# Kernel optimization log

Hardware: AMD Instinct MI355X
Metric: run time of the kernel (lower is better)

## Reference

```python
import jax, jax.numpy as jnp
import numpy as np


def setup_inputs() -> dict:
    key = jax.random.key(0)
    ks = jax.random.split(key, 10)
    B, T, D = 256, 256, 256
    CH, L, K = 128, 3, 10          # chunk_size, levels, conv_size
    H = CH * L                     # hidden_dim = 384
    G = 4 * H + 2 * L              # gate projection width = 1542
    HS = H // 6

    def xavier(k, shape):
        fan_in, fan_out = shape[0], shape[-1]
        lim = np.sqrt(6.0 / (fan_in + fan_out)).astype(np.float32)
        return jax.random.uniform(k, shape, jnp.float32, -lim, lim)

    x = jax.random.normal(ks[0], (B, T, D), jnp.float32)
    lengths = jax.random.randint(ks[1], (B,), 1, T + 1).astype(jnp.int64)
    Wk = xavier(ks[2], (D + 1, G)); bk = jnp.zeros((G,), jnp.float32)
    Wr = xavier(ks[3], (H + 1, G)); br = jnp.zeros((G,), jnp.float32)
    Ws = xavier(ks[4], (H, HS));    bs = jnp.zeros((HS,), jnp.float32)
    Wrs = xavier(ks[5], (HS, H));   brs = jnp.zeros((H,), jnp.float32)
    Wc = xavier(ks[6], (H, H, K)) / np.sqrt(K)  # Conv1d weight (out, in, k)
    bc = jnp.zeros((H,), jnp.float32)
    return {"x": x, "lengths": lengths, "Wk": Wk, "bk": bk, "Wr": Wr,
            "br": br, "Ws": Ws, "bs": bs, "Wrs": Wrs, "brs": brs,
            "Wc": Wc, "bc": bc}


def _cumax_l2r(z):
    return jnp.cumsum(jax.nn.softmax(z, axis=-1), axis=-1)


def _cumax_r2l(z):
    zf = jnp.flip(z, -1)
    return jnp.flip(jnp.cumsum(jax.nn.softmax(zf, axis=-1), axis=-1), -1)


def reference(x, lengths, Wk, bk, Wr, br, Ws, bs, Wrs, brs, Wc, bc):
    B, T, D = x.shape
    H = Wr.shape[0] - 1
    G = Wk.shape[1]
    L = (G - 4 * H) // 2
    CH = H // L
    K = Wc.shape[2]
    ones = jnp.ones((B, 1), x.dtype)

    def step(carry, xt):
        c, h, tmp_h, tmp_dis = carry
        # two linear projections (interval == 1 always)
        xo = (jnp.concatenate([xt, ones], -1) @ Wk + bk
              + jnp.concatenate([h, ones], -1) @ Wr + br)
        fm = _cumax_l2r(xo[:, :L])[:, :, None]          # (B,L,1)
        im = _cumax_r2l(xo[:, L:2 * L])[:, :, None]     # (B,L,1)
        rest = xo[:, 2 * L:].reshape(B, 4 * L, CH)
        f = jax.nn.sigmoid(rest[:, :L])
        i = jax.nn.sigmoid(rest[:, L:2 * L])
        o = jax.nn.sigmoid(rest[:, 2 * L:3 * L])
        c_in = jnp.tanh(rest[:, 3 * L:])
        c_last = c.reshape(B, L, CH)
        ov = fm * im
        c_new = (ov * (f * c_last + i * c_in)
                 + (fm - ov) * c_last + (im - ov) * c_in)
        h_new = (o * jnp.tanh(c_new)).reshape(B, H)
        c_new = c_new.reshape(B, H)
        cur_dis = 1.0 - jnp.mean(fm[..., 0], axis=-1)   # (B,)
        # sliding buffers (K, B, H) and (K, B)
        tmp_h = jnp.concatenate([tmp_h[1:], h_new[None]], 0)
        tmp_dis = jnp.concatenate([tmp_dis[1:], cur_dis[None]], 0)
        # local window attention weights
        ld = jax.nn.softmax(jnp.cumsum(tmp_dis.T, axis=1), axis=1)  # (B,K)
        local_h = tmp_h.transpose(1, 2, 0) * ld[:, None, :]         # (B,H,K)
        theme = jax.nn.sigmoid(
            jax.nn.relu(jnp.mean(local_h, -1) @ Ws + bs) @ Wrs + brs)
        conv = jnp.einsum('bhk,ohk->bo', local_h, Wc) + bc          # valid conv -> len 1
        local_out = theme * conv
        return (c_new, h_new, tmp_h, tmp_dis), (h_new, local_out)

    c0 = jnp.zeros((B, H), x.dtype)
    h0 = jnp.zeros((B, H), x.dtype)
    th0 = jnp.zeros((K, B, H), x.dtype)
    td0 = jnp.zeros((K, B), x.dtype)
    _, (origin_h, loc_h) = jax.lax.scan(step, (c0, h0, th0, td0),
                                        x.transpose(1, 0, 2))
    output = (loc_h + origin_h).transpose(1, 0, 2)   # (B,T,H)
    idx = jnp.clip(lengths, 1, T).astype(jnp.int32) - 1
    last_output = output[jnp.arange(B), idx]
    return (last_output, output)
```

## Files before the change

### kernel.cpp

```cpp
#include <hip/hip_runtime.h>
#include <hip/hip_bf16.h>
#include <cstddef>

#define B_  256
#define T_  256
#define D_  256
#define H_  384
#define G_  1542
#define L_  3
#define CH_ 128
#define K_  10
#define HS_ 64

#define NGRP 16
#define NMEM 16
#define GW   16
#define CPM  24
#define NFR  7
#define PCOLS 112
#define XOLP 114
#define NKC  20
#define W_LDS    (NKC * NFR * 64 * 8 * 2)
#define BIAS_OFF W_LDS
#define UNI_OFF  (W_LDS + 512)
#define HOUT_OFF 12288
#define LDS_BYTES (UNI_OFF + HOUT_OFF + 768)

#define POST_LDS 153600

#define SENT 0xFFFFFFFFFFFFFFFFull

using bf16x8 = __attribute__((ext_vector_type(8))) short;
using f32x4  = __attribute__((ext_vector_type(4))) float;
typedef unsigned long long ull_t;

__device__ __forceinline__ float bf2f(unsigned short s) {
    return __uint_as_float(((unsigned)s) << 16);
}
__device__ __forceinline__ unsigned short f2bf(float f) {
    unsigned u = __float_as_uint(f);
    return (unsigned short)((u + 0x7fffu + ((u >> 16) & 1u)) >> 16);
}
__device__ __forceinline__ float sig_fast(float x) { return 1.f / (1.f + __expf(-x)); }
__device__ __forceinline__ float tanh_fast(float x) {
    float ax = fabsf(x);
    float t = __expf(-2.f * ax);
    float r = (1.f - t) / (1.f + t);
    return copysignf(r, x);
}
__device__ __forceinline__ ull_t ldA(const ull_t* p) {
    return __hip_atomic_load(p, __ATOMIC_RELAXED, __HIP_MEMORY_SCOPE_AGENT);
}

__device__ __forceinline__ int gcol_of(int member, int p) {
    if (p < 6) return p;
    if (p < 102) { int q = p - 6; return 6 + (q / CPM) * H_ + member * CPM + (q % CPM); }
    return -1;
}

__global__ __launch_bounds__(256)
void k_xa(const float* __restrict__ x, unsigned short* __restrict__ xA) {
    __shared__ float xl[64][261];
    const int t = blockIdx.x, bq = blockIdx.y;
    const int b0 = bq * 64, tid = threadIdx.x;
    for (int idx = tid; idx < 4096; idx += 256) {
        int row = idx >> 6, c4 = idx & 63;
        float4 v = *(const float4*)(x + ((size_t)(b0 + row) * T_ + t) * D_ + c4 * 4);
        xl[row][c4 * 4 + 0] = v.x; xl[row][c4 * 4 + 1] = v.y;
        xl[row][c4 * 4 + 2] = v.z; xl[row][c4 * 4 + 3] = v.w;
    }
    __syncthreads();
    for (int idx = tid; idx < 2048; idx += 256) {
        int lane = idx & 63, gl = (idx >> 6) & 3, kc = idx >> 8;
        int brow = gl * 16 + (lane & 15);
        int d = kc * 32 + (lane >> 4) * 8;
        unsigned o[4];
        #pragma unroll
        for (int q = 0; q < 4; ++q)
            o[q] = (unsigned)f2bf(xl[brow][d + 2 * q])
                 | ((unsigned)f2bf(xl[brow][d + 2 * q + 1]) << 16);
        int4 pk = make_int4((int)o[0], (int)o[1], (int)o[2], (int)o[3]);
        ((int4*)xA)[(((size_t)t * 8 + kc) * 16 + (bq * 4 + gl)) * 64 + lane] = pk;
    }
}

__global__ __launch_bounds__(256)
void k_prep(const float* __restrict__ Wk, const float* __restrict__ bk,
            const float* __restrict__ Wr, const float* __restrict__ br,
            const float* __restrict__ Ws, const float* __restrict__ Wrs,
            const float* __restrict__ Wc,
            unsigned short* __restrict__ hbf, unsigned short* __restrict__ Wf,
            unsigned short* __restrict__ Wg, unsigned short* __restrict__ WsT,
            unsigned short* __restrict__ WrsT, float* __restrict__ biasP)
{
    const int bid = blockIdx.x, tid = threadIdx.x;
    if (bid < 2048) {
        ull_t* hb = (ull_t*)hbf;
        int base = bid * 256 + tid;
        #pragma unroll
        for (int j = 0; j < 12; ++j)
            __hip_atomic_store(hb + base + j * 524288, SENT,
                               __ATOMIC_RELAXED, __HIP_MEMORY_SCOPE_AGENT);
    } else if (bid < 2608) {
        int idx = (bid - 2048) * 256 + tid;
        int lane = idx & 63;
        int ni   = (idx >> 6) % NFR;
        int kc   = (idx / (64 * NFR)) % NKC;
        int member = idx / (64 * NFR * NKC);
        int p = ni * 16 + (lane & 15);
        int g = gcol_of(member, p);
        unsigned short out[8];
        #pragma unroll
        for (int j = 0; j < 8; ++j) {
            int k = kc * 32 + (lane >> 4) * 8 + j;
            float v = 0.f;
            if (g >= 0) v = (k < 256) ? Wk[(size_t)k * G_ + g] : Wr[(size_t)(k - 256) * G_ + g];
            out[j] = f2bf(v);
        }
        int4 pk;
        pk.x = (unsigned)out[0] | ((unsigned)out[1] << 16);
        pk.y = (unsigned)out[2] | ((unsigned)out[3] << 16);
        pk.z = (unsigned)out[4] | ((unsigned)out[5] << 16);
        pk.w = (unsigned)out[6] | ((unsigned)out[7] << 16);
        ((int4*)Wf)[idx] = pk;
    } else if (bid < 8368) {
        int idx = (bid - 2608) * 256 + tid;
        int o = idx / (K_ * H_);
        int rem = idx % (K_ * H_);
        int k = rem / H_, h = rem % H_;
        Wg[idx] = f2bf(Wc[((size_t)o * H_ + h) * K_ + k]);
    } else if (bid < 8464) {
        int idx = (bid - 8368) * 256 + tid;
        int jj = idx / H_, k = idx % H_;
        WsT[idx] = f2bf(Ws[(size_t)k * HS_ + jj]);
    } else if (bid < 8560) {
        int idx = (bid - 8464) * 256 + tid;
        int o = idx / HS_, jj = idx % HS_;
        WrsT[idx] = f2bf(Wrs[(size_t)jj * H_ + o]);
    } else {
        int idx = (bid - 8560) * 256 + tid;
        if (idx < NMEM * PCOLS) {
            int member = idx / PCOLS, p = idx % PCOLS;
            int g = gcol_of(member, p);
            biasP[idx] = (g >= 0)
                ? bk[g] + br[g] + Wk[(size_t)256 * G_ + g] + Wr[(size_t)384 * G_ + g] : 0.f;
        }
    }
}

__global__ __launch_bounds__(512, 1)
void k_serial(const unsigned short* __restrict__ xA, const unsigned short* __restrict__ Wf,
              const float* __restrict__ biasP,
              unsigned short* __restrict__ hbf, float* __restrict__ dis)
{
    extern __shared__ char lds_raw[];
    unsigned short* Wl = (unsigned short*)lds_raw;
    float* biasL = (float*)(lds_raw + BIAS_OFF);
    char* uni = lds_raw + UNI_OFF;
    float* xol = (float*)uni;
    unsigned short* hout = (unsigned short*)(uni + HOUT_OFF);
    int4* stage4 = (int4*)uni;
    const bf16x8* stage = (const bf16x8*)uni;

    const int tid = threadIdx.x;
    const int lane = tid & 63, wave = tid >> 6;
    const int group = blockIdx.x & 15, member = blockIdx.x >> 4;
    const int b0 = group * GW;
    const int ni = wave;
    const bool domm = (wave < NFR);

    {
        const int4* src = (const int4*)(Wf + (size_t)member * (NKC * NFR * 64 * 8));
        for (int i = tid; i < W_LDS / 16; i += 512) ((int4*)Wl)[i] = src[i];
        if (tid < PCOLS) biasL[tid] = biasP[member * PCOLS + tid];
    }
    __syncthreads();

    const float bias_a = domm ? biasL[ni * 16 + (lane & 15)] : 0.f;

    const bool hasS = (tid < 384);
    const int skcl = tid >> 6, sln = tid & 63;
    const int stA = skcl * 64 + sln;
    const int stB = (skcl + 6) * 64 + sln;
    const unsigned short* src0 =
        hbf + (size_t)(b0 + (sln & 15)) * H_ + skcl * 32 + (sln >> 4) * 8;

    float c_r0 = 0.f;

    for (int t = 0; t < T_; ++t) {
        bf16x8 xf[8];
        if (domm) {
            #pragma unroll
            for (int kc = 0; kc < 8; ++kc)
                xf[kc] = *((const bf16x8*)(xA
                    + (((size_t)t * 8 + kc) * 16 + group) * 512 + lane * 8));
        }

        f32x4 acc0 = f32x4{bias_a, bias_a, bias_a, bias_a};

        if (t > 0) {
            const size_t toff = (size_t)(t - 1) * B_ * H_;
            const ull_t* pA = (const ull_t*)(src0 + toff);
            const ull_t* pB = (const ull_t*)(src0 + toff + 192);
            ull_t v0 = 0, v1 = 0, v2 = 0, v3 = 0;
            if (hasS) { v0 = ldA(pA); v1 = ldA(pA + 1); v2 = ldA(pB); v3 = ldA(pB + 1); }

            if (domm) {
                #pragma unroll
                for (int kc = 0; kc < 8; ++kc) {
                    bf16x8 w0 = ((const bf16x8*)Wl)[(kc * NFR + ni) * 64 + lane];
                    acc0 = __builtin_amdgcn_mfma_f32_16x16x32_bf16(xf[kc], w0, acc0, 0, 0, 0);
                }
            }

            if (hasS) {
                while ((v0 == SENT) || (v1 == SENT) || (v2 == SENT) || (v3 == SENT)) {
                    v0 = ldA(pA); v1 = ldA(pA + 1); v2 = ldA(pB); v3 = ldA(pB + 1);
                }
                stage4[stA] = make_int4((int)(v0 & 0xffffffffu), (int)(v0 >> 32),
                                        (int)(v1 & 0xffffffffu), (int)(v1 >> 32));
                stage4[stB] = make_int4((int)(v2 & 0xffffffffu), (int)(v2 >> 32),
                                        (int)(v3 & 0xffffffffu), (int)(v3 >> 32));
            }
            __syncthreads();
            if (domm) {
                #pragma unroll
                for (int kcl = 0; kcl < 12; ++kcl) {
                    bf16x8 a0 = stage[kcl * 64 + lane];
                    bf16x8 w0 = ((const bf16x8*)Wl)[((8 + kcl) * NFR + ni) * 64 + lane];
                    acc0 = __builtin_amdgcn_mfma_f32_16x16x32_bf16(a0, w0, acc0, 0, 0, 0);
                }
            }
            __syncthreads();
        } else {
            if (domm) {
                #pragma unroll
                for (int kc = 0; kc < 8; ++kc) {
                    bf16x8 w0 = ((const bf16x8*)Wl)[(kc * NFR + ni) * 64 + lane];
                    acc0 = __builtin_amdgcn_mfma_f32_16x16x32_bf16(xf[kc], w0, acc0, 0, 0, 0);
                }
            }
        }

        if (domm) {
            #pragma unroll
            for (int r = 0; r < 4; ++r)
                xol[((lane >> 4) * 4 + r) * XOLP + ni * 16 + (lane & 15)] = acc0[r];
        }
        __syncthreads();

        if (tid < 384) {
            int b = tid & 15, ch = tid >> 4;
            const float* row = xol + b * XOLP;
            float z0 = row[0], z1 = row[1], z2 = row[2];
            float z3 = row[3], z4 = row[4], z5 = row[5];
            float m1 = fmaxf(fmaxf(z0, z1), z2);
            float e0 = __expf(z0 - m1), e1 = __expf(z1 - m1), e2 = __expf(z2 - m1);
            float inv1 = 1.f / (e0 + e1 + e2);
            float fm0 = e0 * inv1, fm1 = (e0 + e1) * inv1;
            float m2 = fmaxf(fmaxf(z3, z4), z5);
            float f3 = __expf(z3 - m2), f4 = __expf(z4 - m2), f5 = __expf(z5 - m2);
            float inv2 = 1.f / (f3 + f4 + f5);
            float im1 = (f4 + f5) * inv2, im2 = f5 * inv2;

            int hh = member * CPM + ch;
            int l = hh >> 7;
            float fm = (l == 0) ? fm0 : (l == 1) ? fm1 : 1.f;
            float im = (l == 0) ? 1.f : (l == 1) ? im1 : im2;

            float fg = sig_fast(row[6 + ch]);
            float ig = sig_fast(row[6 + CPM + ch]);
            float og = sig_fast(row[6 + 2 * CPM + ch]);
            float ci = tanh_fast(row[6 + 3 * CPM + ch]);

            float ov = fm * im;
            float cn = ov * (fg * c_r0 + ig * ci) + (fm - ov) * c_r0 + (im - ov) * ci;
            float hn = og * tanh_fast(cn);
            c_r0 = cn;

            hout[b * CPM + ch] = f2bf(hn);
            if (member == 0 && ch == 0)
                dis[t * B_ + b0 + b] = 1.f - (fm0 + fm1 + 1.f) * (1.f / 3.f);
        }
        __syncthreads();

        if (tid < 96) {
            int b = tid / 6, jj = tid % 6;
            ull_t v = *(const ull_t*)&hout[b * CPM + jj * 4];
            __hip_atomic_store(
                (ull_t*)(hbf + ((size_t)t * B_ + b0 + b) * H_ + member * CPM + jj * 4),
                v, __ATOMIC_RELAXED, __HIP_MEMORY_SCOPE_AGENT);
        }
    }
}

__global__ __launch_bounds__(512, 1)
void k_post(const unsigned short* __restrict__ hbf, const float* __restrict__ dis,
            const unsigned short* __restrict__ Wg,
            const unsigned short* __restrict__ WsT, const unsigned short* __restrict__ WrsT,
            const float* __restrict__ bs, const float* __restrict__ brs,
            const float* __restrict__ bc, float* __restrict__ out_part)
{
    extern __shared__ char plds[];
    float* ldl = (float*)plds;
    unsigned short* AlB = (unsigned short*)(plds + 10240);
    unsigned short* BlB = (unsigned short*)(plds + 92160);
    unsigned short* hbarL = (unsigned short*)(plds + 10240);
    unsigned short* uL = (unsigned short*)(plds + 65536);

    const int b0 = blockIdx.x * 64;
    const int t0 = blockIdx.y * 4;
    const int tid = threadIdx.x;
    const int wave = tid >> 6, lane = tid & 63;
    const int mh = wave >> 2, nq = wave & 3;

    if (tid < 256) {
        int ti = tid >> 6, bi = tid & 63;
        int t = t0 + ti, b = b0 + bi;
        float s = 0.f, sk[K_];
        #pragma unroll
        for (int k = 0; k < K_; ++k) {
            int tau = t - (K_ - 1) + k;
            float d = (tau >= 0) ? dis[tau * B_ + b] : 0.f;
            s += d; sk[k] = s;
        }
        float m = sk[0];
        #pragma unroll
        for (int k = 1; k < K_; ++k) m = fmaxf(m, sk[k]);
        float sum = 0.f;
        #pragma unroll
        for (int k = 0; k < K_; ++k) { sk[k] = __expf(sk[k] - m); sum += sk[k]; }
        float inv = 1.f / sum;
        #pragma unroll
        for (int k = 0; k < K_; ++k) ldl[ti * 640 + bi * 10 + k] = sk[k] * inv;
    }

    auto loadA = [&](int ch, int4 av[2], bool valid[2]) {
        int k = ch / 12, hb = (ch % 12) * 32;
        #pragma unroll
        for (int i = 0; i < 2; ++i) {
            int s = tid + 512 * i;
            int ti = s >> 8, rem = s & 255;
            int bb = rem >> 2, half = rem & 3;
            int tau = t0 + ti - (K_ - 1) + k;
            valid[i] = (tau >= 0);
            if (valid[i])
                av[i] = *(const int4*)(hbf + ((size_t)tau * B_ + b0 + bb) * H_ + hb + half * 8);
        }
    };
    auto loadB = [&](int ch, int4 bv[3]) {
        #pragma unroll
        for (int q = 0; q < 3; ++q) {
            int idx = q * 512 + tid;
            int row = idx >> 2, half = idx & 3;
            bv[q] = *(const int4*)(Wg + (size_t)row * 3840 + ch * 32 + half * 8);
        }
    };
    auto writeA = [&](int buf, int ch, const int4 av[2], const bool valid[2]) {
        int k = ch / 12;
        #pragma unroll
        for (int i = 0; i < 2; ++i) {
            int s = tid + 512 * i;
            int ti = s >> 8, rem = s & 255;
            int bb = rem >> 2, half = rem & 3;
            int4 pk = make_int4(0, 0, 0, 0);
            if (valid[i]) {
                float l = ldl[ti * 640 + bb * 10 + k];
                unsigned vv[4] = {(unsigned)av[i].x, (unsigned)av[i].y,
                                  (unsigned)av[i].z, (unsigned)av[i].w};
                unsigned o[4];
                #pragma unroll
                for (int q = 0; q < 4; ++q) {
                    float flo = __uint_as_float(vv[q] << 16) * l;
                    float fhi = __uint_as_float(vv[q] & 0xffff0000u) * l;
                    o[q] = (unsigned)f2bf(flo) | ((unsigned)f2bf(fhi) << 16);
                }
                pk = make_int4((int)o[0], (int)o[1], (int)o[2], (int)o[3]);
            }
            *(int4*)&AlB[buf * 10240 + ti * 2560 + bb * 40 + half * 8] = pk;
        }
    };
    auto writeB = [&](int buf, const int4 bv[3]) {
        #pragma unroll
        for (int q = 0; q < 3; ++q) {
            int idx = q * 512 + tid;
            int row = idx >> 2, half = idx & 3;
            *(int4*)&BlB[buf * 15360 + row * 40 + half * 8] = bv[q];
        }
    };

    int4 av[2]; bool avalid[2]; int4 bv[3];
    loadA(0, av, avalid); loadB(0, bv);
    __syncthreads();
    writeA(0, 0, av, avalid); writeB(0, bv);

    f32x4 acc[4][2][6] = {};
    for (int ch = 0; ch < 120; ++ch) {
        int cur = ch & 1;
        bool more = (ch + 1 < 120);
        if (more) { loadA(ch + 1, av, avalid); loadB(ch + 1, bv); }
        __syncthreads();
        if (more) { writeA(cur ^ 1, ch + 1, av, avalid); writeB(cur ^ 1, bv); }

        bf16x8 af[4][2];
        #pragma unroll
        for (int ti = 0; ti < 4; ++ti)
            #pragma unroll
            for (int mi = 0; mi < 2; ++mi)
                af[ti][mi] = *(const bf16x8*)&AlB[cur * 10240 + ti * 2560
                    + (mh * 32 + mi * 16 + (lane & 15)) * 40 + (lane >> 4) * 8];
        #pragma unroll
        for (int ni = 0; ni < 6; ++ni) {
            bf16x8 bfv = *(const bf16x8*)&BlB[cur * 15360
                + (nq * 96 + ni * 16 + (lane & 15)) * 40 + (lane >> 4) * 8];
            #pragma unroll
            for (int ti = 0; ti < 4; ++ti)
                #pragma unroll
                for (int mi = 0; mi < 2; ++mi)
                    acc[ti][mi][ni] = __builtin_amdgcn_mfma_f32_16x16x32_bf16(
                        af[ti][mi], bfv, acc[ti][mi][ni], 0, 0, 0);
        }
    }
    __syncthreads();

    #pragma unroll
    for (int ti = 0; ti < 4; ++ti) {
        const int t = t0 + ti;
        for (int idx = tid; idx < 3072; idx += 512) {
            int bb = idx / 48, h8 = idx % 48;
            float s[8] = {};
            #pragma unroll
            for (int k = 0; k < K_; ++k) {
                int tau = t - (K_ - 1) + k;
                if (tau >= 0) {
                    int4 v = *(const int4*)(hbf + ((size_t)tau * B_ + b0 + bb) * H_ + h8 * 8);
                    float l = ldl[ti * 640 + bb * 10 + k];
                    unsigned vv[4] = {(unsigned)v.x, (unsigned)v.y, (unsigned)v.z, (unsigned)v.w};
                    #pragma unroll
                    for (int q = 0; q < 4; ++q) {
                        s[2 * q]     = fmaf(__uint_as_float(vv[q] << 16), l, s[2 * q]);
                        s[2 * q + 1] = fmaf(__uint_as_float(vv[q] & 0xffff0000u), l, s[2 * q + 1]);
                    }
                }
            }
            unsigned o[4];
            #pragma unroll
            for (int q = 0; q < 4; ++q)
                o[q] = (unsigned)f2bf(s[2 * q] * 0.1f) | ((unsigned)f2bf(s[2 * q + 1] * 0.1f) << 16);
            *(int4*)&hbarL[bb * 400 + h8 * 8] = make_int4((int)o[0], (int)o[1], (int)o[2], (int)o[3]);
        }
        __syncthreads();

        if (wave < 4) {
            f32x4 uacc[4] = {};
            for (int kc = 0; kc < 12; ++kc) {
                bf16x8 a = *(const bf16x8*)&hbarL[(wave * 16 + (lane & 15)) * 400
                                                  + kc * 32 + (lane >> 4) * 8];
                #pragma unroll
                for (int ni = 0; ni < 4; ++ni) {
                    bf16x8 wb = *(const bf16x8*)(WsT + (size_t)(ni * 16 + (lane & 15)) * H_
                                                 + kc * 32 + (lane >> 4) * 8);
                    uacc[ni] = __builtin_amdgcn_mfma_f32_16x16x32_bf16(a, wb, uacc[ni], 0, 0, 0);
                }
            }
            #pragma unroll
            for (int ni = 0; ni < 4; ++ni) {
                float bsv = bs[ni * 16 + (lane & 15)];
                #pragma unroll
                for (int r = 0; r < 4; ++r)
                    uL[(wave * 16 + (lane >> 4) * 4 + r) * 72 + ni * 16 + (lane & 15)] =
                        f2bf(fmaxf(uacc[ni][r] + bsv, 0.f));
            }
        }
        __syncthreads();

        #pragma unroll
        for (int half = 0; half < 2; ++half) {
            f32x4 tacc[2][3] = {};
            #pragma unroll
            for (int kc = 0; kc < 2; ++kc) {
                bf16x8 ua[2];
                #pragma unroll
                for (int mi = 0; mi < 2; ++mi)
                    ua[mi] = *(const bf16x8*)&uL[(mh * 32 + mi * 16 + (lane & 15)) * 72
                                                 + kc * 32 + (lane >> 4) * 8];
                #pragma unroll
                for (int n3 = 0; n3 < 3; ++n3) {
                    int ni = half * 3 + n3;
                    bf16x8 wb = *(const bf16x8*)(WrsT
                        + (size_t)(nq * 96 + ni * 16 + (lane & 15)) * HS_
                        + kc * 32 + (lane >> 4) * 8);
                    #pragma unroll
                    for (int mi = 0; mi < 2; ++mi)
                        tacc[mi][n3] = __builtin_amdgcn_mfma_f32_16x16x32_bf16(
                            ua[mi], wb, tacc[mi][n3], 0, 0, 0);
                }
            }
            #pragma unroll
            for (int mi = 0; mi < 2; ++mi) {
                #pragma unroll
                for (int n3 = 0; n3 < 3; ++n3) {
                    int ni = half * 3 + n3;
                    int o = nq * 96 + ni * 16 + (lane & 15);
                    float brsv = brs[o], bcv = bc[o];
                    int brow0 = b0 + mh * 32 + mi * 16 + ((lane >> 4) << 2);
                    #pragma unroll
                    for (int r = 0; r < 4; ++r) {
                        float th = sig_fast(tacc[mi][n3][r] + brsv);
                        float cv = acc[ti][mi][ni][r] + bcv;
                        float hv = bf2f(hbf[((size_t)t * B_ + brow0 + r) * H_ + o]);
                        out_part[((size_t)(brow0 + r) * T_ + t) * H_ + o] = hv + th * cv;
                    }
                }
            }
        }
        __syncthreads();
    }
}

__global__ void k_last(const int* __restrict__ len_i, const float* __restrict__ out_part,
                       float* __restrict__ last)
{
    int b = blockIdx.x, tid = threadIdx.x;
    bool is64 = (len_i[1] == 0);
    long long v = is64 ? ((const long long*)len_i)[b] : (long long)len_i[b];
    int idx = (int)v;
    idx = max(1, min(T_, idx)) - 1;
    last[(size_t)b * H_ + tid] = out_part[((size_t)b * T_ + idx) * H_ + tid];
}

extern "C" void kernel_launch(void* const* d_in, const int* in_sizes, int n_in,
                              void* d_out, int out_size, void* d_ws, size_t ws_size,
                              hipStream_t stream) {
    const float* x   = (const float*)d_in[0];
    const int*   len = (const int*)d_in[1];
    const float* Wk  = (const float*)d_in[2];
    const float* bk  = (const float*)d_in[3];
    const float* Wr  = (const float*)d_in[4];
    const float* br  = (const float*)d_in[5];
    const float* Ws  = (const float*)d_in[6];
    const float* bs  = (const float*)d_in[7];
    const float* Wrs = (const float*)d_in[8];
    const float* brs = (const float*)d_in[9];
    const float* Wc  = (const float*)d_in[10];
    const float* bc  = (const float*)d_in[11];

    float* out      = (float*)d_out;
    float* last     = out;
    float* out_part = out + (size_t)B_ * H_;

    char* p = (char*)d_ws;
    float*          dis    = (float*)p;          p += (size_t)T_ * B_ * 4;
    unsigned short* xA     = (unsigned short*)p; p += (size_t)T_ * B_ * D_ * 2;
    unsigned short* WfragG = (unsigned short*)p; p += (size_t)NMEM * NKC * NFR * 64 * 8 * 2;
    float*          biasP  = (float*)p;          p += (size_t)NMEM * PCOLS * 4;
    unsigned short* hbf    = (unsigned short*)p; p += (size_t)T_ * B_ * H_ * 2;
    unsigned short* Wg     = (unsigned short*)p; p += (size_t)H_ * K_ * H_ * 2;
    unsigned short* WsT    = (unsigned short*)p; p += (size_t)HS_ * H_ * 2;
    unsigned short* WrsT   = (unsigned short*)p; p += (size_t)H_ * HS_ * 2;

    k_xa  <<<dim3(T_, 4), 256, 0, stream>>>(x, xA);
    k_prep<<<8567, 256, 0, stream>>>(Wk, bk, Wr, br, Ws, Wrs, Wc,
                                     hbf, WfragG, Wg, WsT, WrsT, biasP);

    hipFuncSetAttribute((const void*)k_serial,
                        hipFuncAttributeMaxDynamicSharedMemorySize, LDS_BYTES);
    hipFuncSetAttribute((const void*)k_post,
                        hipFuncAttributeMaxDynamicSharedMemorySize, POST_LDS);

    k_serial<<<NGRP * NMEM, 512, LDS_BYTES, stream>>>(xA, WfragG, biasP, hbf, dis);
    k_post <<<dim3(4, 64), 512, POST_LDS, stream>>>(hbf, dis, Wg, WsT, WrsT, bs, brs, bc, out_part);
    k_last <<<B_, H_, 0, stream>>>(len, out_part, last);
}
```

Baseline: 1.383 ms.

## Split serial MFMA accumulator chain and halve post-kernel time tile

In the serial recurrence kernel, the single MFMA accumulator is split into two interleaved accumulators that are summed at the end, shortening the dependent MFMA chain on the critical path. In the post-processing kernel, each block now covers 2 timesteps instead of 4, doubling the grid to 512 blocks and shrinking LDS and accumulator registers. This should expose more parallelism and occupancy. The cost is that each Wg weight tile is reloaded by twice as many blocks, with less reuse per load.

```diff
diff --git a/kernel.cpp b/kernel.cpp
--- a/kernel.cpp
+++ b/kernel.cpp
@@ -26,7 +26,7 @@
 #define HOUT_OFF 12288
 #define LDS_BYTES (UNI_OFF + HOUT_OFF + 768)
 
-#define POST_LDS 153600
+#define POST_LDS 107520
 
 #define SENT 0xFFFFFFFFFFFFFFFFull
 
@@ -196,7 +196,8 @@
                     + (((size_t)t * 8 + kc) * 16 + group) * 512 + lane * 8));
         }
 
-        f32x4 acc0 = f32x4{bias_a, bias_a, bias_a, bias_a};
+        f32x4 accA = f32x4{bias_a, bias_a, bias_a, bias_a};
+        f32x4 accB = f32x4{0.f, 0.f, 0.f, 0.f};
 
         if (t > 0) {
             const size_t toff = (size_t)(t - 1) * B_ * H_;
@@ -209,7 +210,10 @@
                 #pragma unroll
                 for (int kc = 0; kc < 8; ++kc) {
                     bf16x8 w0 = ((const bf16x8*)Wl)[(kc * NFR + ni) * 64 + lane];
-                    acc0 = __builtin_amdgcn_mfma_f32_16x16x32_bf16(xf[kc], w0, acc0, 0, 0, 0);
+                    if (kc & 1)
+                        accB = __builtin_amdgcn_mfma_f32_16x16x32_bf16(xf[kc], w0, accB, 0, 0, 0);
+                    else
+                        accA = __builtin_amdgcn_mfma_f32_16x16x32_bf16(xf[kc], w0, accA, 0, 0, 0);
                 }
             }
 
@@ -228,7 +232,10 @@
                 for (int kcl = 0; kcl < 12; ++kcl) {
                     bf16x8 a0 = stage[kcl * 64 + lane];
                     bf16x8 w0 = ((const bf16x8*)Wl)[((8 + kcl) * NFR + ni) * 64 + lane];
-                    acc0 = __builtin_amdgcn_mfma_f32_16x16x32_bf16(a0, w0, acc0, 0, 0, 0);
+                    if (kcl & 1)
+                        accB = __builtin_amdgcn_mfma_f32_16x16x32_bf16(a0, w0, accB, 0, 0, 0);
+                    else
+                        accA = __builtin_amdgcn_mfma_f32_16x16x32_bf16(a0, w0, accA, 0, 0, 0);
                 }
             }
             __syncthreads();
@@ -237,7 +244,10 @@
                 #pragma unroll
                 for (int kc = 0; kc < 8; ++kc) {
                     bf16x8 w0 = ((const bf16x8*)Wl)[(kc * NFR + ni) * 64 + lane];
-                    acc0 = __builtin_amdgcn_mfma_f32_16x16x32_bf16(xf[kc], w0, acc0, 0, 0, 0);
+                    if (kc & 1)
+                        accB = __builtin_amdgcn_mfma_f32_16x16x32_bf16(xf[kc], w0, accB, 0, 0, 0);
+                    else
+                        accA = __builtin_amdgcn_mfma_f32_16x16x32_bf16(xf[kc], w0, accA, 0, 0, 0);
                 }
             }
         }
@@ -245,7 +255,7 @@
         if (domm) {
             #pragma unroll
             for (int r = 0; r < 4; ++r)
-                xol[((lane >> 4) * 4 + r) * XOLP + ni * 16 + (lane & 15)] = acc0[r];
+                xol[((lane >> 4) * 4 + r) * XOLP + ni * 16 + (lane & 15)] = accA[r] + accB[r];
         }
         __syncthreads();
 
@@ -303,18 +313,18 @@
 {
     extern __shared__ char plds[];
     float* ldl = (float*)plds;
-    unsigned short* AlB = (unsigned short*)(plds + 10240);
-    unsigned short* BlB = (unsigned short*)(plds + 92160);
-    unsigned short* hbarL = (unsigned short*)(plds + 10240);
-    unsigned short* uL = (unsigned short*)(plds + 65536);
+    unsigned short* AlB = (unsigned short*)(plds + 5120);
+    unsigned short* BlB = (unsigned short*)(plds + 46080);
+    unsigned short* hbarL = (unsigned short*)(plds + 5120);
+    unsigned short* uL = (unsigned short*)(plds + 56320);
 
     const int b0 = blockIdx.x * 64;
-    const int t0 = blockIdx.y * 4;
+    const int t0 = blockIdx.y * 2;
     const int tid = threadIdx.x;
     const int wave = tid >> 6, lane = tid & 63;
     const int mh = wave >> 2, nq = wave & 3;
 
-    if (tid < 256) {
+    if (tid < 128) {
         int ti = tid >> 6, bi = tid & 63;
         int t = t0 + ti, b = b0 + bi;
         float s = 0.f, sk[K_];
@@ -335,18 +345,15 @@
         for (int k = 0; k < K_; ++k) ldl[ti * 640 + bi * 10 + k] = sk[k] * inv;
     }
 
-    auto loadA = [&](int ch, int4 av[2], bool valid[2]) {
+    const int a_ti = tid >> 8, a_rem = tid & 255;
+    const int a_bb = a_rem >> 2, a_half = a_rem & 3;
+
+    auto loadA = [&](int ch, int4& av, bool& valid) {
         int k = ch / 12, hb = (ch % 12) * 32;
-        #pragma unroll
-        for (int i = 0; i < 2; ++i) {
-            int s = tid + 512 * i;
-            int ti = s >> 8, rem = s & 255;
-            int bb = rem >> 2, half = rem & 3;
-            int tau = t0 + ti - (K_ - 1) + k;
-            valid[i] = (tau >= 0);
-            if (valid[i])
-                av[i] = *(const int4*)(hbf + ((size_t)tau * B_ + b0 + bb) * H_ + hb + half * 8);
-        }
+        int tau = t0 + a_ti - (K_ - 1) + k;
+        valid = (tau >= 0);
+        if (valid)
+            av = *(const int4*)(hbf + ((size_t)tau * B_ + b0 + a_bb) * H_ + hb + a_half * 8);
     };
     auto loadB = [&](int ch, int4 bv[3]) {
         #pragma unroll
@@ -356,29 +363,22 @@
             bv[q] = *(const int4*)(Wg + (size_t)row * 3840 + ch * 32 + half * 8);
         }
     };
-    auto writeA = [&](int buf, int ch, const int4 av[2], const bool valid[2]) {
+    auto writeA = [&](int buf, int ch, int4 av, bool valid) {
         int k = ch / 12;
-        #pragma unroll
-        for (int i = 0; i < 2; ++i) {
-            int s = tid + 512 * i;
-            int ti = s >> 8, rem = s & 255;
-            int bb = rem >> 2, half = rem & 3;
-            int4 pk = make_int4(0, 0, 0, 0);
-            if (valid[i]) {
-                float l = ldl[ti * 640 + bb * 10 + k];
-                unsigned vv[4] = {(unsigned)av[i].x, (unsigned)av[i].y,
-                                  (unsigned)av[i].z, (unsigned)av[i].w};
-                unsigned o[4];
-                #pragma unroll
-                for (int q = 0; q < 4; ++q) {
-                    float flo = __uint_as_float(vv[q] << 16) * l;
-                    float fhi = __uint_as_float(vv[q] & 0xffff0000u) * l;
-                    o[q] = (unsigned)f2bf(flo) | ((unsigned)f2bf(fhi) << 16);
-                }
-                pk = make_int4((int)o[0], (int)o[1], (int)o[2], (int)o[3]);
-            }
-            *(int4*)&AlB[buf * 10240 + ti * 2560 + bb * 40 + half * 8] = pk;
-        }
+        int4 pk = make_int4(0, 0, 0, 0);
+        if (valid) {
+            float l = ldl[a_ti * 640 + a_bb * 10 + k];
+            unsigned vv[4] = {(unsigned)av.x, (unsigned)av.y, (unsigned)av.z, (unsigned)av.w};
+            unsigned o[4];
+            #pragma unroll
+            for (int q = 0; q < 4; ++q) {
+                float flo = __uint_as_float(vv[q] << 16) * l;
+                float fhi = __uint_as_float(vv[q] & 0xffff0000u) * l;
+                o[q] = (unsigned)f2bf(flo) | ((unsigned)f2bf(fhi) << 16);
+            }
+            pk = make_int4((int)o[0], (int)o[1], (int)o[2], (int)o[3]);
+        }
+        *(int4*)&AlB[buf * 5120 + a_ti * 2560 + a_bb * 40 + a_half * 8] = pk;
     };
     auto writeB = [&](int buf, const int4 bv[3]) {
         #pragma unroll
@@ -389,12 +389,12 @@
         }
     };
 
-    int4 av[2]; bool avalid[2]; int4 bv[3];
+    int4 av; bool avalid; int4 bv[3];
     loadA(0, av, avalid); loadB(0, bv);
     __syncthreads();
     writeA(0, 0, av, avalid); writeB(0, bv);
 
-    f32x4 acc[4][2][6] = {};
+    f32x4 acc[2][2][6] = {};
     for (int ch = 0; ch < 120; ++ch) {
         int cur = ch & 1;
         bool more = (ch + 1 < 120);
@@ -402,19 +402,19 @@
         __syncthreads();
         if (more) { writeA(cur ^ 1, ch + 1, av, avalid); writeB(cur ^ 1, bv); }
 
-        bf16x8 af[4][2];
-        #pragma unroll
-        for (int ti = 0; ti < 4; ++ti)
+        bf16x8 af[2][2];
+        #pragma unroll
+        for (int ti = 0; ti < 2; ++ti)
             #pragma unroll
             for (int mi = 0; mi < 2; ++mi)
-                af[ti][mi] = *(const bf16x8*)&AlB[cur * 10240 + ti * 2560
+                af[ti][mi] = *(const bf16x8*)&AlB[cur * 5120 + ti * 2560
                     + (mh * 32 + mi * 16 + (lane & 15)) * 40 + (lane >> 4) * 8];
         #pragma unroll
         for (int ni = 0; ni < 6; ++ni) {
             bf16x8 bfv = *(const bf16x8*)&BlB[cur * 15360
                 + (nq * 96 + ni * 16 + (lane & 15)) * 40 + (lane >> 4) * 8];
             #pragma unroll
-            for (int ti = 0; ti < 4; ++ti)
+            for (int ti = 0; ti < 2; ++ti)
                 #pragma unroll
                 for (int mi = 0; mi < 2; ++mi)
                     acc[ti][mi][ni] = __builtin_amdgcn_mfma_f32_16x16x32_bf16(
@@ -424,7 +424,7 @@
     __syncthreads();
 
     #pragma unroll
-    for (int ti = 0; ti < 4; ++ti) {
+    for (int ti = 0; ti < 2; ++ti) {
         const int t = t0 + ti;
         for (int idx = tid; idx < 3072; idx += 512) {
             int bb = idx / 48, h8 = idx % 48;
@@ -569,6 +569,6 @@
                         hipFuncAttributeMaxDynamicSharedMemorySize, POST_LDS);
 
     k_serial<<<NGRP * NMEM, 512, LDS_BYTES, stream>>>(xA, WfragG, biasP, hbf, dis);
-    k_post <<<dim3(4, 64), 512, POST_LDS, stream>>>(hbf, dis, Wg, WsT, WrsT, bs, brs, bc, out_part);
+    k_post <<<dim3(4, 128), 512, POST_LDS, stream>>>(hbf, dis, Wg, WsT, WrsT, bs, brs, bc, out_part);
     k_last <<<B_, H_, 0, stream>>>(len, out_part, last);
 }
```

Measured after the change: 1.304 ms. 5.7% less time.
